# Kernel tuning notes

Hardware: AMD Instinct MI355X
Metric: run time of the kernel (lower is better)

The kernel has to match this reference:

```python
import jax, jax.numpy as jnp
import numpy as np

NEG_SLOPE = 0.2
TEMP = 0.025
EPS = 1e-12

def leaky_relu(x):
    return jnp.where(x >= 0, x, NEG_SLOPE * x)

def setup_inputs() -> dict:
    key = jax.random.key(0)
    k1, k2 = jax.random.split(key)
    B, C, N = 256, 1024, 80
    x = jax.random.normal(k1, (B, C, N), dtype=jnp.float32)
    # Conv1d(C, 1, kernel_size=1) params: weight (1, C, 1) -> flatten to (C,), bias (1,)
    w = jax.random.normal(k2, (C,), dtype=jnp.float32) * (1.0 / np.sqrt(C))
    b = jnp.zeros((1,), dtype=jnp.float32)
    return {"x": x, "w": w, "b": b}

def reference(x, w, b):
    # x: (B, C, N)
    # 1) correlation graph: L2-normalize over channel dim, then Gram matrix over nodes
    norm = jnp.sqrt(jnp.sum(x * x, axis=1, keepdims=True))  # (B,1,N)
    xn = x / jnp.maximum(norm, EPS)
    adj = jnp.einsum('bcn,bcm->bnm', xn, xn)  # (B,N,N)
    # 2) dynamic GCN: x @ adj -> LeakyReLU -> 1x1 conv (C->1) -> LeakyReLU
    h = jnp.einsum('bcn,bnm->bcm', x, adj)  # (B,C,N)
    h = leaky_relu(h)
    s = jnp.einsum('bcn,c->bn', h, w) + b  # (B,N)
    s = leaky_relu(s)
    # 3) temperature-scaled softmax + 1, broadcast multiply
    attn = jax.nn.softmax(s / TEMP, axis=-1) + 1.0  # (B,N)
    return x * attn[:, None, :]  # (B,C,N)
```

## Files before the change

kernel.cpp:

```cpp
#include <hip/hip_runtime.h>

#define CH   1024
#define NPTS 80
#define NEG  0.2f
#define INVTEMP 40.0f

typedef __attribute__((ext_vector_type(8))) short short8;
typedef __attribute__((ext_vector_type(4))) float f32x4;

__device__ __forceinline__ void bsplit(float x, short& hs, short& ls) {
  unsigned u = __builtin_bit_cast(unsigned, x);
  unsigned hb = (u + 0x7fffu + ((u >> 16) & 1u)) >> 16;
  float hf = __builtin_bit_cast(float, hb << 16);
  float r = x - hf;
  unsigned u2 = __builtin_bit_cast(unsigned, r);
  hs = (short)hb;
  ls = (short)((u2 + 0x7fffu + ((u2 >> 16) & 1u)) >> 16);
}

__device__ __forceinline__ float leaky(float v) { return v >= 0.f ? v : NEG * v; }

__launch_bounds__(512, 1)
__global__ void scgcn_fused_kernel(const float* __restrict__ x,
                                   const float* __restrict__ w,
                                   const float* __restrict__ bias,
                                   float* __restrict__ out) {
  __shared__ float G[80][81];
  __shared__ float rn[80];
  __shared__ float ssc[80];
  __shared__ float wl[CH];
  __shared__ __align__(16) short adjh[80][104];
  __shared__ __align__(16) short adjl[80][104];
  __shared__ f32x4 attnv[20];

  const int tid  = threadIdx.x;
  const int lane = tid & 63;
  const int wv   = tid >> 6;
  const int l15  = lane & 15;
  const int g    = lane >> 4;
  const int b    = blockIdx.x;
  const float* __restrict__ xb = x + (size_t)b * (CH * NPTS);

  for (int i = tid; i < 80 * 81; i += 512) (&G[0][0])[i] = 0.f;
  if (tid < 80) ssc[tid] = 0.f;
  for (int i = tid; i < CH; i += 512) wl[i] = w[i];

  f32x4 acc[5][5];
  #pragma unroll
  for (int i = 0; i < 5; ++i)
    #pragma unroll
    for (int j = 0; j < 5; ++j) acc[i][j] = (f32x4){0.f, 0.f, 0.f, 0.f};

  for (int ks = 0; ks < 4; ++ks) {
    const int c0 = wv * 128 + ks * 32 + g * 8;
    short8 fh[5], fl[5];
    #pragma unroll
    for (int t = 0; t < 5; ++t) {
      const int n = 16 * t + l15;
      #pragma unroll
      for (int j = 0; j < 8; ++j) {
        short hs, ls2;
        bsplit(xb[(c0 + j) * NPTS + n], hs, ls2);
        fh[t][j] = hs; fl[t][j] = ls2;
      }
    }
    #pragma unroll
    for (int tn = 0; tn < 5; ++tn)
      #pragma unroll
      for (int tm = 0; tm < 5; ++tm) {
        acc[tn][tm] = __builtin_amdgcn_mfma_f32_16x16x32_bf16(fh[tn], fh[tm], acc[tn][tm], 0, 0, 0);
        acc[tn][tm] = __builtin_amdgcn_mfma_f32_16x16x32_bf16(fh[tn], fl[tm], acc[tn][tm], 0, 0, 0);
        acc[tn][tm] = __builtin_amdgcn_mfma_f32_16x16x32_bf16(fl[tn], fh[tm], acc[tn][tm], 0, 0, 0);
      }
  }
  __syncthreads();
  #pragma unroll
  for (int tn = 0; tn < 5; ++tn)
    #pragma unroll
    for (int tm = 0; tm < 5; ++tm)
      #pragma unroll
      for (int r = 0; r < 4; ++r)
        atomicAdd(&G[16 * tn + 4 * g + r][16 * tm + l15], acc[tn][tm][r]);
  __syncthreads();

  if (tid < 80) rn[tid] = 1.0f / fmaxf(sqrtf(G[tid][tid]), 1e-12f);
  __syncthreads();
  for (int i = tid; i < 80 * 104; i += 512) {
    const int m = i / 104;
    const int n = i - m * 104;
    float v = (n < 80) ? G[n][m] * (rn[n] * rn[m]) : 0.f;
    short hs, ls2; bsplit(v, hs, ls2);
    adjh[m][n] = hs; adjl[m][n] = ls2;
  }
  __syncthreads();

  float sp[5] = {0.f, 0.f, 0.f, 0.f, 0.f};
  for (int chunk = 0; chunk < 2; ++chunk) {
    f32x4 hacc[4][5];
    #pragma unroll
    for (int i = 0; i < 4; ++i)
      #pragma unroll
      for (int j = 0; j < 5; ++j) hacc[i][j] = (f32x4){0.f, 0.f, 0.f, 0.f};

    for (int ksn = 0; ksn < 3; ++ksn) {
      const int nb = 32 * ksn + 8 * g;
      short8 bh[5], bl[5];
      #pragma unroll
      for (int tm = 0; tm < 5; ++tm) {
        bh[tm] = *reinterpret_cast<const short8*>(&adjh[16 * tm + l15][nb]);
        bl[tm] = *reinterpret_cast<const short8*>(&adjl[16 * tm + l15][nb]);
      }
      #pragma unroll
      for (int t4 = 0; t4 < 4; ++t4) {
        const int ct = wv * 8 + chunk * 4 + t4;
        short8 ah, al;
        if (nb < 80) {
          const float* p = xb + (16 * ct + l15) * NPTS + nb;
          f32x4 va = *reinterpret_cast<const f32x4*>(p);
          f32x4 vb = *reinterpret_cast<const f32x4*>(p + 4);
          #pragma unroll
          for (int j = 0; j < 4; ++j) { short hs, ls2; bsplit(va[j], hs, ls2); ah[j] = hs; al[j] = ls2; }
          #pragma unroll
          for (int j = 0; j < 4; ++j) { short hs, ls2; bsplit(vb[j], hs, ls2); ah[4 + j] = hs; al[4 + j] = ls2; }
        } else {
          ah = (short8){0,0,0,0,0,0,0,0};
          al = (short8){0,0,0,0,0,0,0,0};
        }
        #pragma unroll
        for (int tm = 0; tm < 5; ++tm) {
          hacc[t4][tm] = __builtin_amdgcn_mfma_f32_16x16x32_bf16(ah, bh[tm], hacc[t4][tm], 0, 0, 0);
          hacc[t4][tm] = __builtin_amdgcn_mfma_f32_16x16x32_bf16(ah, bl[tm], hacc[t4][tm], 0, 0, 0);
          hacc[t4][tm] = __builtin_amdgcn_mfma_f32_16x16x32_bf16(al, bh[tm], hacc[t4][tm], 0, 0, 0);
        }
      }
    }
    #pragma unroll
    for (int t4 = 0; t4 < 4; ++t4) {
      const int cb = 16 * (wv * 8 + chunk * 4 + t4) + 4 * g;
      #pragma unroll
      for (int r = 0; r < 4; ++r) {
        const float wc = wl[cb + r];
        #pragma unroll
        for (int tm = 0; tm < 5; ++tm) sp[tm] += leaky(hacc[t4][tm][r]) * wc;
      }
    }
  }
  #pragma unroll
  for (int tm = 0; tm < 5; ++tm) {
    float v = sp[tm];
    v += __shfl_xor(v, 16);
    v += __shfl_xor(v, 32);
    if (g == 0) atomicAdd(&ssc[16 * tm + l15], v);
  }
  __syncthreads();

  if (wv == 0) {
    const float b0 = bias[0];
    float v0 = leaky(ssc[lane] + b0) * INVTEMP;
    float v1 = -3.0e38f;
    if (lane < 16) v1 = leaky(ssc[64 + lane] + b0) * INVTEMP;
    float mx = fmaxf(v0, v1);
    #pragma unroll
    for (int off = 32; off >= 1; off >>= 1) mx = fmaxf(mx, __shfl_xor(mx, off));
    float e0 = expf(v0 - mx);
    float e1 = (lane < 16) ? expf(v1 - mx) : 0.f;
    float sum = e0 + e1;
    #pragma unroll
    for (int off = 32; off >= 1; off >>= 1) sum += __shfl_xor(sum, off);
    const float inv = 1.0f / sum;
    ssc[lane] = e0 * inv + 1.0f;
    if (lane < 16) ssc[64 + lane] = e1 * inv + 1.0f;
  }
  __syncthreads();
  if (tid < 20) {
    f32x4 a = { ssc[4 * tid], ssc[4 * tid + 1], ssc[4 * tid + 2], ssc[4 * tid + 3] };
    attnv[tid] = a;
  }
  __syncthreads();

  float* __restrict__ ob = out + (size_t)b * (CH * NPTS);
  const f32x4* xv = reinterpret_cast<const f32x4*>(xb);
  f32x4* ov = reinterpret_cast<f32x4*>(ob);
  #pragma unroll 4
  for (int i = tid; i < (CH * NPTS) / 4; i += 512) {
    f32x4 v = xv[i];
    f32x4 a = attnv[i % 20];
    v[0] *= a[0]; v[1] *= a[1]; v[2] *= a[2]; v[3] *= a[3];
    ov[i] = v;
  }
}

extern "C" void kernel_launch(void* const* d_in, const int* in_sizes, int n_in,
                              void* d_out, int out_size, void* d_ws, size_t ws_size,
                              hipStream_t stream) {
  const float* x    = (const float*)d_in[0];
  const float* w    = (const float*)d_in[1];
  const float* bias = (const float*)d_in[2];
  float* out        = (float*)d_out;
  scgcn_fused_kernel<<<256, 512, 0, stream>>>(x, w, bias, out);
}
```

Baseline: 247.4 us.

## Split fused kernel into gram, adjacency, gemm and scale kernels over channel slices

```diff
diff --git a/kernel.cpp b/kernel.cpp
--- a/kernel.cpp
+++ b/kernel.cpp
@@ -4,6 +4,7 @@
 #define NPTS 80
 #define NEG  0.2f
 #define INVTEMP 40.0f
+#define NSLICE 4
 
 typedef __attribute__((ext_vector_type(8))) short short8;
 typedef __attribute__((ext_vector_type(4))) float f32x4;
@@ -19,6 +20,232 @@
 }
 
 __device__ __forceinline__ float leaky(float v) { return v >= 0.f ? v : NEG * v; }
+
+__launch_bounds__(256)
+__global__ void k1_gram(const float* __restrict__ x, float* __restrict__ Gpart) {
+  __shared__ float G[80][81];
+  const int tid  = threadIdx.x;
+  const int lane = tid & 63;
+  const int wv   = tid >> 6;
+  const int l15  = lane & 15;
+  const int g    = lane >> 4;
+  const int slice = blockIdx.x & (NSLICE - 1);
+  const int b     = blockIdx.x >> 2;
+  const float* __restrict__ xb = x + (size_t)b * (CH * NPTS);
+
+  for (int i = tid; i < 80 * 81; i += 256) (&G[0][0])[i] = 0.f;
+
+  f32x4 acc[5][5];
+  #pragma unroll
+  for (int i = 0; i < 5; ++i)
+    #pragma unroll
+    for (int j = 0; j < 5; ++j) acc[i][j] = (f32x4){0.f, 0.f, 0.f, 0.f};
+
+  for (int ks2 = 0; ks2 < 2; ++ks2) {
+    const int c0 = slice * 256 + wv * 64 + ks2 * 32 + g * 8;
+    short8 fh[5], fl[5];
+    #pragma unroll
+    for (int t = 0; t < 5; ++t) {
+      const int n = 16 * t + l15;
+      #pragma unroll
+      for (int j = 0; j < 8; ++j) {
+        short hs, ls2;
+        bsplit(xb[(c0 + j) * NPTS + n], hs, ls2);
+        fh[t][j] = hs; fl[t][j] = ls2;
+      }
+    }
+    #pragma unroll
+    for (int tn = 0; tn < 5; ++tn)
+      #pragma unroll
+      for (int tm = 0; tm < 5; ++tm) {
+        acc[tn][tm] = __builtin_amdgcn_mfma_f32_16x16x32_bf16(fh[tn], fh[tm], acc[tn][tm], 0, 0, 0);
+        acc[tn][tm] = __builtin_amdgcn_mfma_f32_16x16x32_bf16(fh[tn], fl[tm], acc[tn][tm], 0, 0, 0);
+        acc[tn][tm] = __builtin_amdgcn_mfma_f32_16x16x32_bf16(fl[tn], fh[tm], acc[tn][tm], 0, 0, 0);
+      }
+  }
+  __syncthreads();
+  #pragma unroll
+  for (int tn = 0; tn < 5; ++tn)
+    #pragma unroll
+    for (int tm = 0; tm < 5; ++tm)
+      #pragma unroll
+      for (int r = 0; r < 4; ++r)
+        atomicAdd(&G[16 * tn + 4 * g + r][16 * tm + l15], acc[tn][tm][r]);
+  __syncthreads();
+
+  float* __restrict__ gp = Gpart + ((size_t)slice * 256 + b) * 6400;
+  for (int i = tid; i < 6400; i += 256) gp[i] = G[i / 80][i % 80];
+}
+
+__launch_bounds__(256)
+__global__ void k2_adj(const float* __restrict__ Gpart,
+                       unsigned short* __restrict__ adjh,
+                       unsigned short* __restrict__ adjl,
+                       float* __restrict__ s) {
+  __shared__ float Gs[80][80];
+  __shared__ float rn[80];
+  const int tid = threadIdx.x;
+  const int b = blockIdx.x;
+  if (tid < 80) s[b * 80 + tid] = 0.f;
+  for (int i = tid; i < 6400; i += 256) {
+    float v = 0.f;
+    #pragma unroll
+    for (int sl = 0; sl < NSLICE; ++sl)
+      v += Gpart[((size_t)sl * 256 + b) * 6400 + i];
+    (&Gs[0][0])[i] = v;
+  }
+  __syncthreads();
+  if (tid < 80) rn[tid] = 1.0f / fmaxf(sqrtf(Gs[tid][tid]), 1e-12f);
+  __syncthreads();
+  for (int i = tid; i < 80 * 96; i += 256) {
+    const int m = i / 96;
+    const int n = i - m * 96;
+    float v = (n < 80) ? Gs[m][n] * (rn[m] * rn[n]) : 0.f;
+    short hs, ls2; bsplit(v, hs, ls2);
+    adjh[(size_t)b * 7680 + i] = (unsigned short)hs;
+    adjl[(size_t)b * 7680 + i] = (unsigned short)ls2;
+  }
+}
+
+__launch_bounds__(256)
+__global__ void k3_gemm2(const float* __restrict__ x,
+                         const unsigned short* __restrict__ adjh_g,
+                         const unsigned short* __restrict__ adjl_g,
+                         const float* __restrict__ w,
+                         float* __restrict__ s) {
+  __shared__ __align__(16) short adjh[80][104];
+  __shared__ __align__(16) short adjl[80][104];
+  __shared__ float wl[256];
+  __shared__ float ssc[80];
+  const int tid  = threadIdx.x;
+  const int lane = tid & 63;
+  const int wv   = tid >> 6;
+  const int l15  = lane & 15;
+  const int g    = lane >> 4;
+  const int slice = blockIdx.x & (NSLICE - 1);
+  const int b     = blockIdx.x >> 2;
+  const float* __restrict__ xb = x + (size_t)b * (CH * NPTS);
+
+  for (int i = tid; i < 960; i += 256) {
+    const int row = i / 12;
+    const int c8  = (i - row * 12) * 8;
+    short8 vh = *reinterpret_cast<const short8*>(adjh_g + (size_t)b * 7680 + row * 96 + c8);
+    short8 vl = *reinterpret_cast<const short8*>(adjl_g + (size_t)b * 7680 + row * 96 + c8);
+    *reinterpret_cast<short8*>(&adjh[row][c8]) = vh;
+    *reinterpret_cast<short8*>(&adjl[row][c8]) = vl;
+  }
+  wl[tid] = w[slice * 256 + tid];
+  if (tid < 80) ssc[tid] = 0.f;
+  __syncthreads();
+
+  f32x4 hacc[4][5];
+  #pragma unroll
+  for (int i = 0; i < 4; ++i)
+    #pragma unroll
+    for (int j = 0; j < 5; ++j) hacc[i][j] = (f32x4){0.f, 0.f, 0.f, 0.f};
+
+  for (int ksn = 0; ksn < 3; ++ksn) {
+    const int nb = 32 * ksn + 8 * g;
+    short8 bh[5], bl[5];
+    #pragma unroll
+    for (int tm = 0; tm < 5; ++tm) {
+      bh[tm] = *reinterpret_cast<const short8*>(&adjh[16 * tm + l15][nb]);
+      bl[tm] = *reinterpret_cast<const short8*>(&adjl[16 * tm + l15][nb]);
+    }
+    #pragma unroll
+    for (int t4 = 0; t4 < 4; ++t4) {
+      const int row = slice * 256 + wv * 64 + t4 * 16 + l15;
+      short8 ah, al;
+      if (nb < 80) {
+        const float* p = xb + row * NPTS + nb;
+        f32x4 va = *reinterpret_cast<const f32x4*>(p);
+        f32x4 vb = *reinterpret_cast<const f32x4*>(p + 4);
+        #pragma unroll
+        for (int j = 0; j < 4; ++j) { short hs, ls2; bsplit(va[j], hs, ls2); ah[j] = hs; al[j] = ls2; }
+        #pragma unroll
+        for (int j = 0; j < 4; ++j) { short hs, ls2; bsplit(vb[j], hs, ls2); ah[4 + j] = hs; al[4 + j] = ls2; }
+      } else {
+        ah = (short8){0,0,0,0,0,0,0,0};
+        al = (short8){0,0,0,0,0,0,0,0};
+      }
+      #pragma unroll
+      for (int tm = 0; tm < 5; ++tm) {
+        hacc[t4][tm] = __builtin_amdgcn_mfma_f32_16x16x32_bf16(ah, bh[tm], hacc[t4][tm], 0, 0, 0);
+        hacc[t4][tm] = __builtin_amdgcn_mfma_f32_16x16x32_bf16(ah, bl[tm], hacc[t4][tm], 0, 0, 0);
+        hacc[t4][tm] = __builtin_amdgcn_mfma_f32_16x16x32_bf16(al, bh[tm], hacc[t4][tm], 0, 0, 0);
+      }
+    }
+  }
+
+  float sp[5] = {0.f, 0.f, 0.f, 0.f, 0.f};
+  #pragma unroll
+  for (int t4 = 0; t4 < 4; ++t4) {
+    const int cbl = wv * 64 + t4 * 16 + 4 * g;
+    #pragma unroll
+    for (int r = 0; r < 4; ++r) {
+      const float wc = wl[cbl + r];
+      #pragma unroll
+      for (int tm = 0; tm < 5; ++tm) sp[tm] += leaky(hacc[t4][tm][r]) * wc;
+    }
+  }
+  #pragma unroll
+  for (int tm = 0; tm < 5; ++tm) {
+    float v = sp[tm];
+    v += __shfl_xor(v, 16);
+    v += __shfl_xor(v, 32);
+    if (g == 0) atomicAdd(&ssc[16 * tm + l15], v);
+  }
+  __syncthreads();
+  if (tid < 80) atomicAdd(&s[b * 80 + tid], ssc[tid]);
+}
+
+__launch_bounds__(256)
+__global__ void k5_scale(const float* __restrict__ x,
+                         const float* __restrict__ s,
+                         const float* __restrict__ bias,
+                         float* __restrict__ out) {
+  __shared__ float att[80];
+  __shared__ f32x4 attnv[20];
+  const int tid = threadIdx.x;
+  const int b = blockIdx.x / 10;
+  const int chunk = blockIdx.x - b * 10;
+
+  if (tid < 64) {
+    const int lane = tid;
+    const float b0 = bias[0];
+    float v0 = leaky(s[b * 80 + lane] + b0) * INVTEMP;
+    float v1 = -3.0e38f;
+    if (lane < 16) v1 = leaky(s[b * 80 + 64 + lane] + b0) * INVTEMP;
+    float mx = fmaxf(v0, v1);
+    #pragma unroll
+    for (int off = 32; off >= 1; off >>= 1) mx = fmaxf(mx, __shfl_xor(mx, off));
+    float e0 = expf(v0 - mx);
+    float e1 = (lane < 16) ? expf(v1 - mx) : 0.f;
+    float sum = e0 + e1;
+    #pragma unroll
+    for (int off = 32; off >= 1; off >>= 1) sum += __shfl_xor(sum, off);
+    const float inv = 1.0f / sum;
+    att[lane] = e0 * inv + 1.0f;
+    if (lane < 16) att[64 + lane] = e1 * inv + 1.0f;
+  }
+  __syncthreads();
+  if (tid < 20) {
+    f32x4 a = { att[4 * tid], att[4 * tid + 1], att[4 * tid + 2], att[4 * tid + 3] };
+    attnv[tid] = a;
+  }
+  __syncthreads();
+
+  const f32x4* __restrict__ xv = reinterpret_cast<const f32x4*>(x + (size_t)b * (CH * NPTS));
+  f32x4* __restrict__ ov = reinterpret_cast<f32x4*>(out + (size_t)b * (CH * NPTS));
+  #pragma unroll
+  for (int k = 0; k < 8; ++k) {
+    const int e4 = chunk * 2048 + k * 256 + tid;
+    f32x4 v = xv[e4];
+    f32x4 a = attnv[e4 % 20];
+    v[0] *= a[0]; v[1] *= a[1]; v[2] *= a[2]; v[3] *= a[3];
+    ov[e4] = v;
+  }
+}
 
 __launch_bounds__(512, 1)
 __global__ void scgcn_fused_kernel(const float* __restrict__ x,
@@ -197,5 +424,24 @@
   const float* w    = (const float*)d_in[1];
   const float* bias = (const float*)d_in[2];
   float* out        = (float*)d_out;
-  scgcn_fused_kernel<<<256, 512, 0, stream>>>(x, w, bias, out);
-}
+
+  const size_t gpart_bytes = (size_t)NSLICE * 256 * 6400 * sizeof(float);
+  const size_t adj_bytes   = (size_t)256 * 7680 * sizeof(unsigned short);
+  const size_t s_bytes     = (size_t)256 * 80 * sizeof(float);
+  const size_t need = gpart_bytes + 2 * adj_bytes + s_bytes;
+
+  if (ws_size >= need) {
+    char* p = (char*)d_ws;
+    float* Gpart = (float*)p;                 p += gpart_bytes;
+    unsigned short* adjh = (unsigned short*)p; p += adj_bytes;
+    unsigned short* adjl = (unsigned short*)p; p += adj_bytes;
+    float* sws = (float*)p;
+
+    k1_gram<<<NSLICE * 256, 256, 0, stream>>>(x, Gpart);
+    k2_adj<<<256, 256, 0, stream>>>(Gpart, adjh, adjl, sws);
+    k3_gemm2<<<NSLICE * 256, 256, 0, stream>>>(x, adjh, adjl, w, sws);
+    k5_scale<<<256 * 10, 256, 0, stream>>>(x, sws, bias, out);
+  } else {
+    scgcn_fused_kernel<<<256, 512, 0, stream>>>(x, w, bias, out);
+  }
+}
```

After: 330.7 us. 1.34x slower.

## Stage bf16 hi/lo split of x through shared memory for Gram phase

Applied to the files above, without the earlier changes.

```diff
diff --git a/kernel.cpp b/kernel.cpp
--- a/kernel.cpp
+++ b/kernel.cpp
@@ -7,6 +7,7 @@
 
 typedef __attribute__((ext_vector_type(8))) short short8;
 typedef __attribute__((ext_vector_type(4))) float f32x4;
+typedef __attribute__((ext_vector_type(4))) unsigned u32x4;
 
 __device__ __forceinline__ void bsplit(float x, short& hs, short& ls) {
   unsigned u = __builtin_bit_cast(unsigned, x);
@@ -18,6 +19,24 @@
   ls = (short)((u2 + 0x7fffu + ((u2 >> 16) & 1u)) >> 16);
 }
 
+__device__ __forceinline__ unsigned packhl(float x) {
+  short hs, ls; bsplit(x, hs, ls);
+  return ((unsigned)(unsigned short)hs << 16) | (unsigned)(unsigned short)ls;
+}
+
+__device__ __forceinline__ void unpack8(u32x4 q0, u32x4 q1, short8& fh, short8& fl) {
+  union { unsigned u[4]; short8 s; } a, b;
+  a.u[0] = (q0[0] >> 16) | (q0[1] & 0xffff0000u);
+  a.u[1] = (q0[2] >> 16) | (q0[3] & 0xffff0000u);
+  a.u[2] = (q1[0] >> 16) | (q1[1] & 0xffff0000u);
+  a.u[3] = (q1[2] >> 16) | (q1[3] & 0xffff0000u);
+  b.u[0] = (q0[0] & 0xffffu) | (q0[1] << 16);
+  b.u[1] = (q0[2] & 0xffffu) | (q0[3] << 16);
+  b.u[2] = (q1[0] & 0xffffu) | (q1[1] << 16);
+  b.u[3] = (q1[2] & 0xffffu) | (q1[3] << 16);
+  fh = a.s; fl = b.s;
+}
+
 __device__ __forceinline__ float leaky(float v) { return v >= 0.f ? v : NEG * v; }
 
 __launch_bounds__(512, 1)
@@ -25,13 +44,16 @@
                                    const float* __restrict__ w,
                                    const float* __restrict__ bias,
                                    float* __restrict__ out) {
+  __shared__ __align__(16) char smem[83200];
   __shared__ float G[80][81];
   __shared__ float rn[80];
   __shared__ float ssc[80];
   __shared__ float wl[CH];
-  __shared__ __align__(16) short adjh[80][104];
-  __shared__ __align__(16) short adjl[80][104];
   __shared__ f32x4 attnv[20];
+
+  unsigned* __restrict__ xP = (unsigned*)smem;
+  short (*adjh)[104] = (short (*)[104])smem;
+  short (*adjl)[104] = (short (*)[104])(smem + 16640);
 
   const int tid  = threadIdx.x;
   const int lane = tid & 63;
@@ -51,19 +73,32 @@
     #pragma unroll
     for (int j = 0; j < 5; ++j) acc[i][j] = (f32x4){0.f, 0.f, 0.f, 0.f};
 
-  for (int ks = 0; ks < 4; ++ks) {
-    const int c0 = wv * 128 + ks * 32 + g * 8;
+  for (int chunk = 0; chunk < 4; ++chunk) {
+    for (int k = 0; k < 10; ++k) {
+      const int U  = tid + 512 * k;
+      const int n  = U % 80;
+      const int c0 = (U / 80) * 4;
+      const float* p = xb + (size_t)(chunk * 256 + c0) * NPTS + n;
+      u32x4 pk;
+      pk[0] = packhl(p[0 * NPTS]);
+      pk[1] = packhl(p[1 * NPTS]);
+      pk[2] = packhl(p[2 * NPTS]);
+      pk[3] = packhl(p[3 * NPTS]);
+      *reinterpret_cast<u32x4*>(&xP[n * 260 + c0]) = pk;
+    }
+    __syncthreads();
+
     short8 fh[5], fl[5];
+    const int cbase = wv * 32 + g * 8;
     #pragma unroll
     for (int t = 0; t < 5; ++t) {
       const int n = 16 * t + l15;
-      #pragma unroll
-      for (int j = 0; j < 8; ++j) {
-        short hs, ls2;
-        bsplit(xb[(c0 + j) * NPTS + n], hs, ls2);
-        fh[t][j] = hs; fl[t][j] = ls2;
-      }
-    }
+      u32x4 q0 = *reinterpret_cast<const u32x4*>(&xP[n * 260 + cbase]);
+      u32x4 q1 = *reinterpret_cast<const u32x4*>(&xP[n * 260 + cbase + 4]);
+      unpack8(q0, q1, fh[t], fl[t]);
+    }
+    __syncthreads();
+
     #pragma unroll
     for (int tn = 0; tn < 5; ++tn)
       #pragma unroll
@@ -73,6 +108,7 @@
         acc[tn][tm] = __builtin_amdgcn_mfma_f32_16x16x32_bf16(fl[tn], fh[tm], acc[tn][tm], 0, 0, 0);
       }
   }
+
   __syncthreads();
   #pragma unroll
   for (int tn = 0; tn < 5; ++tn)
```

Result: slower. 274.9 us (+11.1%).

## Stage x chunks into LDS via direct global-to-LDS loads and split scaling kernel

Applied to the files above, without the earlier changes.

```diff
diff --git a/kernel.cpp b/kernel.cpp
--- a/kernel.cpp
+++ b/kernel.cpp
@@ -20,18 +20,25 @@
 
 __device__ __forceinline__ float leaky(float v) { return v >= 0.f ? v : NEG * v; }
 
+__device__ __forceinline__ void dma16(const void* g, void* l) {
+  __builtin_amdgcn_global_load_lds(
+      (const __attribute__((address_space(1))) unsigned*)g,
+      (__attribute__((address_space(3))) unsigned*)l,
+      16, 0, 0);
+}
+
 __launch_bounds__(512, 1)
-__global__ void scgcn_fused_kernel(const float* __restrict__ x,
-                                   const float* __restrict__ w,
-                                   const float* __restrict__ bias,
-                                   float* __restrict__ out) {
+__global__ void scgcn_main_kernel(const float* __restrict__ x,
+                                  const float* __restrict__ w,
+                                  const float* __restrict__ bias,
+                                  float* __restrict__ attn_ws) {
+  __shared__ __align__(16) float xstage[256 * 80];
   __shared__ float G[80][81];
   __shared__ float rn[80];
   __shared__ float ssc[80];
   __shared__ float wl[CH];
   __shared__ __align__(16) short adjh[80][104];
   __shared__ __align__(16) short adjl[80][104];
-  __shared__ f32x4 attnv[20];
 
   const int tid  = threadIdx.x;
   const int lane = tid & 63;
@@ -51,19 +58,32 @@
     #pragma unroll
     for (int j = 0; j < 5; ++j) acc[i][j] = (f32x4){0.f, 0.f, 0.f, 0.f};
 
-  for (int ks = 0; ks < 4; ++ks) {
-    const int c0 = wv * 128 + ks * 32 + g * 8;
+  for (int chunk = 0; chunk < 4; ++chunk) {
+    {
+      const char* gsrc = (const char*)(xb + (size_t)chunk * 256 * NPTS);
+      char* lbase = (char*)xstage;
+      #pragma unroll
+      for (int i = 0; i < 10; ++i) {
+        const int off = (wv * 10 + i) * 1024;
+        dma16(gsrc + off + lane * 16, lbase + off);
+      }
+    }
+    __syncthreads();
+
     short8 fh[5], fl[5];
+    const int cbase = wv * 32 + g * 8;
     #pragma unroll
     for (int t = 0; t < 5; ++t) {
       const int n = 16 * t + l15;
       #pragma unroll
       for (int j = 0; j < 8; ++j) {
         short hs, ls2;
-        bsplit(xb[(c0 + j) * NPTS + n], hs, ls2);
+        bsplit(xstage[(cbase + j) * 80 + n], hs, ls2);
         fh[t][j] = hs; fl[t][j] = ls2;
       }
     }
+    __syncthreads();
+
     #pragma unroll
     for (int tn = 0; tn < 5; ++tn)
       #pragma unroll
@@ -73,6 +93,7 @@
         acc[tn][tm] = __builtin_amdgcn_mfma_f32_16x16x32_bf16(fl[tn], fh[tm], acc[tn][tm], 0, 0, 0);
       }
   }
+
   __syncthreads();
   #pragma unroll
   for (int tn = 0; tn < 5; ++tn)
@@ -95,10 +116,21 @@
   __syncthreads();
 
   float sp[5] = {0.f, 0.f, 0.f, 0.f, 0.f};
-  for (int chunk = 0; chunk < 2; ++chunk) {
-    f32x4 hacc[4][5];
-    #pragma unroll
-    for (int i = 0; i < 4; ++i)
+  for (int chunk = 0; chunk < 4; ++chunk) {
+    {
+      const char* gsrc = (const char*)(xb + (size_t)chunk * 256 * NPTS);
+      char* lbase = (char*)xstage;
+      #pragma unroll
+      for (int i = 0; i < 10; ++i) {
+        const int off = (wv * 10 + i) * 1024;
+        dma16(gsrc + off + lane * 16, lbase + off);
+      }
+    }
+    __syncthreads();
+
+    f32x4 hacc[2][5];
+    #pragma unroll
+    for (int i = 0; i < 2; ++i)
       #pragma unroll
       for (int j = 0; j < 5; ++j) hacc[i][j] = (f32x4){0.f, 0.f, 0.f, 0.f};
 
@@ -111,11 +143,11 @@
         bl[tm] = *reinterpret_cast<const short8*>(&adjl[16 * tm + l15][nb]);
       }
       #pragma unroll
-      for (int t4 = 0; t4 < 4; ++t4) {
-        const int ct = wv * 8 + chunk * 4 + t4;
+      for (int ct = 0; ct < 2; ++ct) {
+        const int row = (wv * 2 + ct) * 16 + l15;
         short8 ah, al;
         if (nb < 80) {
-          const float* p = xb + (16 * ct + l15) * NPTS + nb;
+          const float* p = &xstage[row * 80 + nb];
           f32x4 va = *reinterpret_cast<const f32x4*>(p);
           f32x4 vb = *reinterpret_cast<const f32x4*>(p + 4);
           #pragma unroll
@@ -128,23 +160,26 @@
         }
         #pragma unroll
         for (int tm = 0; tm < 5; ++tm) {
-          hacc[t4][tm] = __builtin_amdgcn_mfma_f32_16x16x32_bf16(ah, bh[tm], hacc[t4][tm], 0, 0, 0);
-          hacc[t4][tm] = __builtin_amdgcn_mfma_f32_16x16x32_bf16(ah, bl[tm], hacc[t4][tm], 0, 0, 0);
-          hacc[t4][tm] = __builtin_amdgcn_mfma_f32_16x16x32_bf16(al, bh[tm], hacc[t4][tm], 0, 0, 0);
+          hacc[ct][tm] = __builtin_amdgcn_mfma_f32_16x16x32_bf16(ah, bh[tm], hacc[ct][tm], 0, 0, 0);
+          hacc[ct][tm] = __builtin_amdgcn_mfma_f32_16x16x32_bf16(ah, bl[tm], hacc[ct][tm], 0, 0, 0);
+          hacc[ct][tm] = __builtin_amdgcn_mfma_f32_16x16x32_bf16(al, bh[tm], hacc[ct][tm], 0, 0, 0);
         }
       }
     }
-    #pragma unroll
-    for (int t4 = 0; t4 < 4; ++t4) {
-      const int cb = 16 * (wv * 8 + chunk * 4 + t4) + 4 * g;
+
+    #pragma unroll
+    for (int ct = 0; ct < 2; ++ct) {
+      const int cb = chunk * 256 + (wv * 2 + ct) * 16 + 4 * g;
       #pragma unroll
       for (int r = 0; r < 4; ++r) {
         const float wc = wl[cb + r];
         #pragma unroll
-        for (int tm = 0; tm < 5; ++tm) sp[tm] += leaky(hacc[t4][tm][r]) * wc;
-      }
-    }
-  }
+        for (int tm = 0; tm < 5; ++tm) sp[tm] += leaky(hacc[ct][tm][r]) * wc;
+      }
+    }
+    __syncthreads();
+  }
+
   #pragma unroll
   for (int tm = 0; tm < 5; ++tm) {
     float v = sp[tm];
@@ -168,25 +203,32 @@
     #pragma unroll
     for (int off = 32; off >= 1; off >>= 1) sum += __shfl_xor(sum, off);
     const float inv = 1.0f / sum;
-    ssc[lane] = e0 * inv + 1.0f;
-    if (lane < 16) ssc[64 + lane] = e1 * inv + 1.0f;
-  }
-  __syncthreads();
-  if (tid < 20) {
-    f32x4 a = { ssc[4 * tid], ssc[4 * tid + 1], ssc[4 * tid + 2], ssc[4 * tid + 3] };
-    attnv[tid] = a;
-  }
-  __syncthreads();
-
-  float* __restrict__ ob = out + (size_t)b * (CH * NPTS);
-  const f32x4* xv = reinterpret_cast<const f32x4*>(xb);
-  f32x4* ov = reinterpret_cast<f32x4*>(ob);
-  #pragma unroll 4
-  for (int i = tid; i < (CH * NPTS) / 4; i += 512) {
-    f32x4 v = xv[i];
-    f32x4 a = attnv[i % 20];
+    attn_ws[b * 80 + lane] = e0 * inv + 1.0f;
+    if (lane < 16) attn_ws[b * 80 + 64 + lane] = e1 * inv + 1.0f;
+  }
+}
+
+__launch_bounds__(256)
+__global__ void scgcn_scale_kernel(const float* __restrict__ x,
+                                   const float* __restrict__ attn_ws,
+                                   float* __restrict__ out) {
+  __shared__ f32x4 attnv[20];
+  const int tid   = threadIdx.x;
+  const int b     = blockIdx.x >> 3;
+  const int chunk = blockIdx.x & 7;
+
+  if (tid < 20) attnv[tid] = reinterpret_cast<const f32x4*>(attn_ws + b * 80)[tid];
+  __syncthreads();
+
+  const f32x4* __restrict__ xv = reinterpret_cast<const f32x4*>(x + (size_t)b * (CH * NPTS));
+  f32x4* __restrict__ ov = reinterpret_cast<f32x4*>(out + (size_t)b * (CH * NPTS));
+  #pragma unroll
+  for (int k = 0; k < 10; ++k) {
+    const int e4 = chunk * 2560 + k * 256 + tid;
+    f32x4 v = xv[e4];
+    f32x4 a = attnv[e4 % 20];
     v[0] *= a[0]; v[1] *= a[1]; v[2] *= a[2]; v[3] *= a[3];
-    ov[i] = v;
+    ov[e4] = v;
   }
 }
 
@@ -197,5 +239,8 @@
   const float* w    = (const float*)d_in[1];
   const float* bias = (const float*)d_in[2];
   float* out        = (float*)d_out;
-  scgcn_fused_kernel<<<256, 512, 0, stream>>>(x, w, bias, out);
-}
+  float* attn_ws    = (float*)d_ws;
+
+  scgcn_main_kernel<<<256, 512, 0, stream>>>(x, w, bias, attn_ws);
+  scgcn_scale_kernel<<<256 * 8, 256, 0, stream>>>(x, attn_ws, out);
+}
```

Result: no change. 252.3 us (+2.0%).
